# Optimization experiments

Measured on AMD Instinct MI355X. Metric: run time of the kernel, lower is better.

The kernel has to match this reference:

```python
import jax, jax.numpy as jnp
import numpy as np

B, P = 32768, 8
AFF_V, MAT_V, TASK_V, OBJ_V, ST_V = 16, 16, 16, 64, 32
AFF_D = MAT_D = TASK_D = OBJ_D = ST_D = 64
PART_D, OBJ_ENC_D = 256, 256


def setup_inputs() -> dict:
    key = jax.random.key(0)
    ks = jax.random.split(key, 16)
    inp = {
        "aff_idx": jax.random.randint(ks[0], (B, P), 0, AFF_V),
        "mat_idx": jax.random.randint(ks[1], (B, P), 0, MAT_V),
        "task_idx": jax.random.randint(ks[2], (B,), 0, TASK_V),
        "obj_idx": jax.random.randint(ks[3], (B,), 0, OBJ_V),
        "state_idx": jax.random.randint(ks[4], (B,), 0, ST_V),
        "aff_emb": jax.random.normal(ks[5], (AFF_V, AFF_D), jnp.float32),
        "mat_emb": jax.random.normal(ks[6], (MAT_V, MAT_D), jnp.float32),
        "task_emb": jax.random.normal(ks[7], (TASK_V, TASK_D), jnp.float32),
        "obj_emb": jax.random.normal(ks[8], (OBJ_V, OBJ_D), jnp.float32),
        "state_emb": jax.random.normal(ks[9], (ST_V, ST_D), jnp.float32),
        "W_part": jax.random.normal(ks[10], (PART_D, AFF_D + MAT_D), jnp.float32) * 0.05,
        "b_part": jax.random.normal(ks[11], (PART_D,), jnp.float32) * 0.05,
        "W_obj": jax.random.normal(ks[12], (OBJ_ENC_D, TASK_D + OBJ_D + ST_D + PART_D), jnp.float32) * 0.05,
        "b_obj": jax.random.normal(ks[13], (OBJ_ENC_D,), jnp.float32) * 0.05,
    }
    return inp


def reference(aff_idx, mat_idx, task_idx, obj_idx, state_idx,
              aff_emb, mat_emb, task_emb, obj_emb, state_emb,
              W_part, b_part, W_obj, b_obj):
    # Per-part: gather two embeddings, concat, linear, relu  -> [B, P, PART_D]
    part_in = jnp.concatenate([aff_emb[aff_idx], mat_emb[mat_idx]], axis=-1)  # [B,P,128]
    part_enc = jax.nn.relu(jnp.einsum('bpk,ok->bpo', part_in, W_part) + b_part)
    # Max-pool over parts (torch.max values)
    parts_pooled = jnp.max(part_enc, axis=1)  # [B, PART_D]
    # Object-level: concat categorical embeddings with pooled part encoding
    obj_in = jnp.concatenate([task_emb[task_idx], obj_emb[obj_idx],
                              state_emb[state_idx], parts_pooled], axis=-1)  # [B,448]
    return jax.nn.relu(obj_in @ W_obj.T + b_obj)  # [B, OBJ_ENC_D]
```

## Files before the change

### kernel.cpp

```cpp
#include <hip/hip_runtime.h>
#include <hip/hip_bf16.h>


typedef float          f32x4  __attribute__((ext_vector_type(4)));
typedef short          s16x8  __attribute__((ext_vector_type(8)));
typedef unsigned short u16x8  __attribute__((ext_vector_type(8)));

__device__ __forceinline__ unsigned short f2bf_rne(float x) {
    unsigned u = __float_as_uint(x);
    u += 0x7FFFu + ((u >> 16) & 1u);
    return (unsigned short)(u >> 16);
}

#define WS_PART_TABLE 0
#define WS_WP2T       131072
#define WS_TT         262144
#define WS_TO         278528
#define WS_TS         344064

__global__ __launch_bounds__(256) void precompute_kernel(
    const float* __restrict__ aff_emb, const float* __restrict__ mat_emb,
    const float* __restrict__ task_emb, const float* __restrict__ obj_emb,
    const float* __restrict__ state_emb,
    const float* __restrict__ W_part, const float* __restrict__ b_part,
    const float* __restrict__ W_obj, const float* __restrict__ b_obj,
    char* __restrict__ ws)
{
    short* part_table = (short*)(ws + WS_PART_TABLE);
    short* wp2t       = (short*)(ws + WS_WP2T);
    float* Tt         = (float*)(ws + WS_TT);
    float* To         = (float*)(ws + WS_TO);
    float* Ts         = (float*)(ws + WS_TS);

    int bid = blockIdx.x, tid = threadIdx.x;
    __shared__ float rowv[128];

    if (bid < 256) {
        int a = bid >> 4, m = bid & 15;
        if (tid < 64)       rowv[tid] = aff_emb[a*64 + tid];
        else if (tid < 128) rowv[tid] = mat_emb[m*64 + (tid-64)];
        __syncthreads();
        float s = b_part[tid];
        const float* w = &W_part[tid*128];
        #pragma unroll
        for (int k = 0; k < 128; k += 4) {
            float4 wv = *(const float4*)&w[k];
            s += rowv[k]*wv.x + rowv[k+1]*wv.y + rowv[k+2]*wv.z + rowv[k+3]*wv.w;
        }
        part_table[bid*256 + tid] = (short)f2bf_rne(fmaxf(s, 0.f));
    } else if (bid < 368) {
        int rr = bid - 256;
        const float* emb; int koff; float* dst;
        if (rr < 16)      { emb = &task_emb[rr*64];        koff = 0;   dst = &Tt[rr*256]; }
        else if (rr < 80) { emb = &obj_emb[(rr-16)*64];    koff = 64;  dst = &To[(rr-16)*256]; }
        else              { emb = &state_emb[(rr-80)*64];  koff = 128; dst = &Ts[(rr-80)*256]; }
        if (tid < 64) rowv[tid] = emb[tid];
        __syncthreads();
        float s = (rr < 16) ? b_obj[tid] : 0.f;
        const float* w = &W_obj[tid*448 + koff];
        #pragma unroll
        for (int k = 0; k < 64; k += 4) {
            float4 wv = *(const float4*)&w[k];
            s += rowv[k]*wv.x + rowv[k+1]*wv.y + rowv[k+2]*wv.z + rowv[k+3]*wv.w;
        }
        dst[tid] = s;
    } else {
        int n = bid - 368;
        wp2t[n*256 + tid] = (short)f2bf_rne(W_obj[n*448 + 192 + tid]);
    }
}

__global__ __launch_bounds__(256) void main_kernel(
    const int* __restrict__ aff_idx, const int* __restrict__ mat_idx,
    const int* __restrict__ task_idx, const int* __restrict__ obj_idx,
    const int* __restrict__ state_idx,
    const char* __restrict__ ws, float* __restrict__ out)
{
    const short* part_table = (const short*)(ws + WS_PART_TABLE);
    const short* wp2t       = (const short*)(ws + WS_WP2T);
    const float* Tt         = (const float*)(ws + WS_TT);
    const float* To         = (const float*)(ws + WS_TO);
    const float* Ts         = (const float*)(ws + WS_TS);

    __shared__ short pooled[16*264];
    __shared__ int   pair_s[16*8];
    __shared__ int   tos_s[48];

    int tid  = threadIdx.x;
    int wave = tid >> 6, lane = tid & 63;
    int l15 = lane & 15, l4 = lane >> 4;

    int row0 = blockIdx.x * 16;

    if (tid < 128) {
        int r = tid >> 3, j = tid & 7;
        int a = aff_idx[(row0+r)*8 + j];
        int m = mat_idx[(row0+r)*8 + j];
        pair_s[r*8 + j] = (a*16 + m) * 256;
    } else if (tid < 176) {
        int u = tid - 128;
        int r = u & 15, wh = u >> 4;
        int row = row0 + r;
        int v = (wh == 0) ? task_idx[row] : (wh == 1) ? obj_idx[row] : state_idx[row];
        tos_s[wh*16 + r] = v;
    }
    __syncthreads();

    {
        int r = tid >> 4, e = tid & 15;
        u16x8 mx0 = (u16x8)(0), mx1 = (u16x8)(0);
        #pragma unroll
        for (int p = 0; p < 8; ++p) {
            int off = pair_s[r*8 + p] + e*16;
            u16x8 v0 = *(const u16x8*)&part_table[off];
            u16x8 v1 = *(const u16x8*)&part_table[off + 8];
            mx0 = __builtin_elementwise_max(mx0, v0);
            mx1 = __builtin_elementwise_max(mx1, v1);
        }
        *(u16x8*)&pooled[r*264 + e*16]     = mx0;
        *(u16x8*)&pooled[r*264 + e*16 + 8] = mx1;
    }
    __syncthreads();

    f32x4 acc[4];
    #pragma unroll
    for (int nt = 0; nt < 4; ++nt) acc[nt] = (f32x4){0.f, 0.f, 0.f, 0.f};

    const short* bbase = &wp2t[(wave*64 + l15)*256 + l4*8];
    #pragma unroll
    for (int ks = 0; ks < 8; ++ks) {
        s16x8 af = *(const s16x8*)&pooled[l15*264 + ks*32 + l4*8];
        #pragma unroll
        for (int nt = 0; nt < 4; ++nt) {
            s16x8 bf = *(const s16x8*)&bbase[nt*16*256 + ks*32];
            acc[nt] = __builtin_amdgcn_mfma_f32_16x16x32_bf16(af, bf, acc[nt], 0, 0, 0);
        }
    }

    #pragma unroll
    for (int nt = 0; nt < 4; ++nt) {
        int col = wave*64 + nt*16 + l15;
        #pragma unroll
        for (int reg = 0; reg < 4; ++reg) {
            int rl  = l4*4 + reg;
            int row = row0 + rl;
            int t = tos_s[rl], o = tos_s[16 + rl], s = tos_s[32 + rl];
            float v = acc[nt][reg] + Tt[t*256 + col] + To[o*256 + col] + Ts[s*256 + col];
            out[row*256 + col] = fmaxf(v, 0.f);
        }
    }
}

extern "C" void kernel_launch(void* const* d_in, const int* in_sizes, int n_in,
                              void* d_out, int out_size, void* d_ws, size_t ws_size,
                              hipStream_t stream) {
    const int*   aff_idx   = (const int*)d_in[0];
    const int*   mat_idx   = (const int*)d_in[1];
    const int*   task_idx  = (const int*)d_in[2];
    const int*   obj_idx   = (const int*)d_in[3];
    const int*   state_idx = (const int*)d_in[4];
    const float* aff_emb   = (const float*)d_in[5];
    const float* mat_emb   = (const float*)d_in[6];
    const float* task_emb  = (const float*)d_in[7];
    const float* obj_emb   = (const float*)d_in[8];
    const float* state_emb = (const float*)d_in[9];
    const float* W_part    = (const float*)d_in[10];
    const float* b_part    = (const float*)d_in[11];
    const float* W_obj     = (const float*)d_in[12];
    const float* b_obj     = (const float*)d_in[13];

    precompute_kernel<<<624, 256, 0, stream>>>(
        aff_emb, mat_emb, task_emb, obj_emb, state_emb,
        W_part, b_part, W_obj, b_obj, (char*)d_ws);

    main_kernel<<<2048, 256, 0, stream>>>(
        aff_idx, mat_idx, task_idx, obj_idx, state_idx,
        (const char*)d_ws, (float*)d_out);
}
```

Before: 133.6 us.

## Use persistent 1024-thread blocks with LDS-staged bias tables and register-resident weights

```diff
diff --git a/kernel.cpp b/kernel.cpp
--- a/kernel.cpp
+++ b/kernel.cpp
@@ -5,6 +5,7 @@
 typedef float          f32x4  __attribute__((ext_vector_type(4)));
 typedef short          s16x8  __attribute__((ext_vector_type(8)));
 typedef unsigned short u16x8  __attribute__((ext_vector_type(8)));
+typedef unsigned short u16x4  __attribute__((ext_vector_type(4)));
 
 __device__ __forceinline__ unsigned short f2bf_rne(float x) {
     unsigned u = __float_as_uint(x);
@@ -70,7 +71,7 @@
     }
 }
 
-__global__ __launch_bounds__(256) void main_kernel(
+__global__ __launch_bounds__(1024, 4) void main_kernel(
     const int* __restrict__ aff_idx, const int* __restrict__ mat_idx,
     const int* __restrict__ task_idx, const int* __restrict__ obj_idx,
     const int* __restrict__ state_idx,
@@ -78,76 +79,81 @@
 {
     const short* part_table = (const short*)(ws + WS_PART_TABLE);
     const short* wp2t       = (const short*)(ws + WS_WP2T);
-    const float* Tt         = (const float*)(ws + WS_TT);
-    const float* To         = (const float*)(ws + WS_TO);
-    const float* Ts         = (const float*)(ws + WS_TS);
 
+    __shared__ float catL[112*256];
     __shared__ short pooled[16*264];
-    __shared__ int   pair_s[16*8];
-    __shared__ int   tos_s[48];
+    __shared__ int   pair_all[128*8];
+    __shared__ int   tos_all[3*128];
 
     int tid  = threadIdx.x;
-    int wave = tid >> 6, lane = tid & 63;
-    int l15 = lane & 15, l4 = lane >> 4;
+    int wv   = tid >> 6, lane = tid & 63;
+    int l15  = lane & 15, l4 = lane >> 4;
+    int row0 = blockIdx.x * 128;
 
-    int row0 = blockIdx.x * 16;
+    {
+        const float4* csrc = (const float4*)(ws + WS_TT);
+        float4* cdst = (float4*)catL;
+        #pragma unroll
+        for (int k = 0; k < 7; ++k)
+            cdst[tid + k*1024] = csrc[tid + k*1024];
+    }
+    {
+        int a = aff_idx[row0*8 + tid];
+        int m = mat_idx[row0*8 + tid];
+        pair_all[tid] = (a*16 + m) * 256;
+    }
+    if (tid < 384) {
+        int wh = tid >> 7, r = tid & 127;
+        const int* p = (wh == 0) ? task_idx : (wh == 1) ? obj_idx : state_idx;
+        tos_all[wh*128 + r] = p[row0 + r];
+    }
 
-    if (tid < 128) {
-        int r = tid >> 3, j = tid & 7;
-        int a = aff_idx[(row0+r)*8 + j];
-        int m = mat_idx[(row0+r)*8 + j];
-        pair_s[r*8 + j] = (a*16 + m) * 256;
-    } else if (tid < 176) {
-        int u = tid - 128;
-        int r = u & 15, wh = u >> 4;
-        int row = row0 + r;
-        int v = (wh == 0) ? task_idx[row] : (wh == 1) ? obj_idx[row] : state_idx[row];
-        tos_s[wh*16 + r] = v;
-    }
+    s16x8 bfrag[8];
+    #pragma unroll
+    for (int ks = 0; ks < 8; ++ks)
+        bfrag[ks] = *(const s16x8*)&wp2t[(wv*16 + l15)*256 + ks*32 + l4*8];
+
     __syncthreads();
 
-    {
-        int r = tid >> 4, e = tid & 15;
-        u16x8 mx0 = (u16x8)(0), mx1 = (u16x8)(0);
+    int pr = tid >> 6, pe = tid & 63;
+    u16x4 pl[8];
+    #pragma unroll
+    for (int p = 0; p < 8; ++p)
+        pl[p] = *(const u16x4*)&part_table[pair_all[pr*8 + p] + pe*4];
+
+    for (int t = 0; t < 8; ++t) {
+        u16x4 mx = pl[0];
         #pragma unroll
-        for (int p = 0; p < 8; ++p) {
-            int off = pair_s[r*8 + p] + e*16;
-            u16x8 v0 = *(const u16x8*)&part_table[off];
-            u16x8 v1 = *(const u16x8*)&part_table[off + 8];
-            mx0 = __builtin_elementwise_max(mx0, v0);
-            mx1 = __builtin_elementwise_max(mx1, v1);
+        for (int p = 1; p < 8; ++p) mx = __builtin_elementwise_max(mx, pl[p]);
+        *(u16x4*)&pooled[pr*264 + pe*4] = mx;
+        __syncthreads();
+
+        if (t < 7) {
+            #pragma unroll
+            for (int p = 0; p < 8; ++p)
+                pl[p] = *(const u16x4*)&part_table[pair_all[((t+1)*16 + pr)*8 + p] + pe*4];
         }
-        *(u16x8*)&pooled[r*264 + e*16]     = mx0;
-        *(u16x8*)&pooled[r*264 + e*16 + 8] = mx1;
-    }
-    __syncthreads();
 
-    f32x4 acc[4];
-    #pragma unroll
-    for (int nt = 0; nt < 4; ++nt) acc[nt] = (f32x4){0.f, 0.f, 0.f, 0.f};
+        f32x4 acc = (f32x4){0.f, 0.f, 0.f, 0.f};
+        #pragma unroll
+        for (int ks = 0; ks < 8; ++ks) {
+            s16x8 af = *(const s16x8*)&pooled[l15*264 + ks*32 + l4*8];
+            acc = __builtin_amdgcn_mfma_f32_16x16x32_bf16(af, bfrag[ks], acc, 0, 0, 0);
+        }
 
-    const short* bbase = &wp2t[(wave*64 + l15)*256 + l4*8];
-    #pragma unroll
-    for (int ks = 0; ks < 8; ++ks) {
-        s16x8 af = *(const s16x8*)&pooled[l15*264 + ks*32 + l4*8];
-        #pragma unroll
-        for (int nt = 0; nt < 4; ++nt) {
-            s16x8 bf = *(const s16x8*)&bbase[nt*16*256 + ks*32];
-            acc[nt] = __builtin_amdgcn_mfma_f32_16x16x32_bf16(af, bf, acc[nt], 0, 0, 0);
-        }
-    }
-
-    #pragma unroll
-    for (int nt = 0; nt < 4; ++nt) {
-        int col = wave*64 + nt*16 + l15;
+        int col = wv*16 + l15;
         #pragma unroll
         for (int reg = 0; reg < 4; ++reg) {
-            int rl  = l4*4 + reg;
-            int row = row0 + rl;
-            int t = tos_s[rl], o = tos_s[16 + rl], s = tos_s[32 + rl];
-            float v = acc[nt][reg] + Tt[t*256 + col] + To[o*256 + col] + Ts[s*256 + col];
-            out[row*256 + col] = fmaxf(v, 0.f);
+            int rl = l4*4 + reg;
+            int ti = tos_all[t*16 + rl];
+            int oi = tos_all[128 + t*16 + rl];
+            int si = tos_all[256 + t*16 + rl];
+            float v = acc[reg] + catL[ti*256 + col]
+                               + catL[(16 + oi)*256 + col]
+                               + catL[(80 + si)*256 + col];
+            out[(row0 + t*16 + rl)*256 + col] = fmaxf(v, 0.f);
         }
+        __syncthreads();
     }
 }
 
@@ -173,7 +179,7 @@
         aff_emb, mat_emb, task_emb, obj_emb, state_emb,
         W_part, b_part, W_obj, b_obj, (char*)d_ws);
 
-    main_kernel<<<2048, 256, 0, stream>>>(
+    main_kernel<<<256, 1024, 0, stream>>>(
         aff_idx, mat_idx, task_idx, obj_idx, state_idx,
         (const char*)d_ws, (float*)d_out);
 }
```

Result: faster. 113.0 us (-15.4%).
